# Optimization experiments

Measured on AMD Instinct MI355X. Metric: run time of the kernel, lower is better.

Reference implementation:

```python
import jax, jax.numpy as jnp
import numpy as np

B0, C0, H0, W0 = 2, 64, 48, 48
BR, DI, NS, RK, K = 128, 128, 16, 4, 4
EPS = 1e-5


def _bn_relu(x, g, b):
    # eval-mode BatchNorm2d (running mean 0, var 1) followed by ReLU; x is NCHW
    return jax.nn.relu(x * (g / jnp.sqrt(1.0 + EPS))[None, :, None, None] + b[None, :, None, None])


def _c1(x, w):
    # 1x1 conv, w: (O, C, 1, 1)
    return jnp.einsum('bchw,oc->bohw', x, w[:, :, 0, 0])


def _avgpool(x, k, s, p):
    # torch AvgPool2d with count_include_pad=True -> divide by k*k
    y = jax.lax.reduce_window(x, 0.0, jax.lax.add, (1, 1, k, k), (1, 1, s, s), ((0, 0), (0, 0), (p, p), (p, p)))
    return y / float(k * k)


def _resize(x, h, w):
    # bilinear, align_corners=False (half-pixel), NCHW
    return jax.image.resize(x, (x.shape[0], x.shape[1], h, w), 'bilinear')


def _pappm(x, s0_g, s0_b, s0_w, s1_g, s1_b, s1_w, s2_g, s2_b, s2_w, s3_g, s3_b, s3_w, s4_g, s4_b, s4_w, comp_g, comp_b, comp_w, sc_g, sc_b, sc_w):
    h, w = x.shape[2], x.shape[3]
    x0 = _c1(_bn_relu(x, s0_g, s0_b), s0_w)
    y1 = _c1(_bn_relu(_avgpool(x, 3, 1, 1), s1_g, s1_b), s1_w) + x0  # stride-1 pool keeps size
    y2 = _resize(_c1(_bn_relu(_avgpool(x, 5, 2, 2), s2_g, s2_b), s2_w), h, w) + x0
    y3 = _resize(_c1(_bn_relu(_avgpool(x, 9, 4, 4), s3_g, s3_b), s3_w), h, w) + x0
    y4 = _c1(_bn_relu(x.mean((2, 3), keepdims=True), s4_g, s4_b), s4_w) + x0  # 1x1 -> broadcast
    cat = jnp.concatenate([x0, y1, y2, y3, y4], axis=1)  # (B, 5*BR, H, W)
    comp = jax.lax.conv_general_dilated(_bn_relu(cat, comp_g, comp_b), comp_w, (1, 1), ((1, 1), (1, 1)), dimension_numbers=('NCHW', 'OIHW', 'NCHW'))
    return comp + _c1(_bn_relu(x, sc_g, sc_b), sc_w)


def _ss2d(xin, in_proj_w, dw_w, dw_b, x_proj_w, dt_w, dt_b, A_logs, Ds, ln_g, ln_b, out_proj_w):
    # xin: (B, H, W, d_model)
    Bb, Hh, Ww, _ = xin.shape
    xz = xin @ in_proj_w.T                      # (B,H,W,2*DI)
    xc, z = jnp.split(xz, 2, axis=-1)
    xc = jnp.transpose(xc, (0, 3, 1, 2))        # (B,DI,H,W)
    xc = jax.lax.conv_general_dilated(xc, dw_w, (1, 1), ((1, 1), (1, 1)), dimension_numbers=('NCHW', 'OIHW', 'NCHW'), feature_group_count=DI)
    xc = jax.nn.silu(xc + dw_b[None, :, None, None])
    L = Hh * Ww
    x_hw = xc.reshape(Bb, DI, L)
    x_wh = jnp.transpose(xc, (0, 1, 3, 2)).reshape(Bb, DI, L)
    xs = jnp.stack([x_hw, x_wh, x_hw[:, :, ::-1], x_wh[:, :, ::-1]], axis=1)  # (B,K,DI,L)
    x_dbl = jnp.einsum('bkdl,kcd->bkcl', xs, x_proj_w)
    dts, Bm, Cm = jnp.split(x_dbl, [RK, RK + NS], axis=2)  # (B,K,RK,L),(B,K,NS,L),(B,K,NS,L)
    delta = jax.nn.softplus(jnp.einsum('bkrl,kdr->bkdl', dts, dt_w) + dt_b[None, :, :, None])  # (B,K,DI,L)
    A = -jnp.exp(A_logs).reshape(K, DI, NS)
    a = jnp.exp(delta[..., None] * A[None, :, :, None, :])                    # (B,K,DI,L,NS)
    bu = (delta * xs)[..., None] * jnp.transpose(Bm, (0, 1, 3, 2))[:, :, None]  # (B,K,DI,L,NS)

    def comb(e1, e2):
        a1, b1 = e1
        a2, b2 = e2
        return a2 * a1, a2 * b1 + b2

    _, hst = jax.lax.associative_scan(comb, (a, bu), axis=3)  # h_t = a_t*h_{t-1} + b_t
    y = jnp.einsum('bkdln,bknl->bkdl', hst, Cm) + xs * Ds.reshape(K, DI)[None, :, :, None]
    inv = y[:, 2:4][:, :, :, ::-1]
    y3 = jnp.transpose(y[:, 1].reshape(Bb, DI, Ww, Hh), (0, 1, 3, 2)).reshape(Bb, DI, L)
    y4 = jnp.transpose(inv[:, 1].reshape(Bb, DI, Ww, Hh), (0, 1, 3, 2)).reshape(Bb, DI, L)
    ys = jnp.transpose(y[:, 0] + inv[:, 0] + y3 + y4, (0, 2, 1)).reshape(Bb, Hh, Ww, DI)
    mu = ys.mean(-1, keepdims=True)
    var = jnp.mean((ys - mu) ** 2, -1, keepdims=True)
    yn = (ys - mu) / jnp.sqrt(var + EPS) * ln_g + ln_b
    return (yn * jax.nn.silu(z)) @ out_proj_w.T  # (B,H,W,d_model)


def setup_inputs():
    key = jax.random.key(0)
    ks = iter(jax.random.split(key, 32))
    nrm = lambda shp, s: jax.random.normal(next(ks), shp, jnp.float32) * s
    d = {}
    d['x'] = nrm((B0, C0, H0, W0), 1.0)
    for nm in ['s0', 's1', 's2', 's3', 's4']:
        d[nm + '_g'] = jnp.ones((C0,), jnp.float32)
        d[nm + '_b'] = jnp.zeros((C0,), jnp.float32)
        d[nm + '_w'] = nrm((BR, C0, 1, 1), (2.0 / C0) ** 0.5)
    d['comp_g'] = jnp.ones((5 * BR,), jnp.float32)
    d['comp_b'] = jnp.zeros((5 * BR,), jnp.float32)
    d['comp_w'] = nrm((C0, 5 * BR, 3, 3), (2.0 / (5 * BR * 9)) ** 0.5)
    d['sc_g'] = jnp.ones((C0,), jnp.float32)
    d['sc_b'] = jnp.zeros((C0,), jnp.float32)
    d['sc_w'] = nrm((C0, C0, 1, 1), (2.0 / C0) ** 0.5)
    d['in_proj_w'] = nrm((2 * DI, C0), C0 ** -0.5)
    d['dw_w'] = nrm((DI, 1, 3, 3), 0.3)
    d['dw_b'] = jnp.zeros((DI,), jnp.float32)
    d['x_proj_w'] = nrm((K, RK + 2 * NS, DI), DI ** -0.5)
    d['dt_w'] = nrm((K, DI, RK), RK ** -0.5)
    d['dt_b'] = jnp.log(jnp.expm1(jnp.asarray(0.01, jnp.float32))) * jnp.ones((K, DI), jnp.float32)
    d['A_logs'] = jnp.tile(jnp.log(jnp.arange(1, NS + 1, dtype=jnp.float32))[None], (K * DI, 1))
    d['Ds'] = jnp.ones((K * DI,), jnp.float32)
    d['ln_g'] = jnp.ones((DI,), jnp.float32)
    d['ln_b'] = jnp.zeros((DI,), jnp.float32)
    d['out_proj_w'] = nrm((C0, DI), DI ** -0.5)
    d['fc1_w'] = nrm((BR, C0, 1, 1), C0 ** -0.5)
    d['fc1_b'] = jnp.zeros((BR,), jnp.float32)
    d['fc2_w'] = nrm((C0, BR, 1, 1), BR ** -0.5)
    d['fc2_b'] = jnp.zeros((C0,), jnp.float32)
    return d


def reference(x, s0_g, s0_b, s0_w, s1_g, s1_b, s1_w, s2_g, s2_b, s2_w, s3_g, s3_b, s3_w, s4_g, s4_b, s4_w, comp_g, comp_b, comp_w, sc_g, sc_b, sc_w, in_proj_w, dw_w, dw_b, x_proj_w, dt_w, dt_b, A_logs, Ds, ln_g, ln_b, out_proj_w, fc1_w, fc1_b, fc2_w, fc2_b):
    p = _pappm(x, s0_g, s0_b, s0_w, s1_g, s1_b, s1_w, s2_g, s2_b, s2_w, s3_g, s3_b, s3_w, s4_g, s4_b, s4_w, comp_g, comp_b, comp_w, sc_g, sc_b, sc_w)
    a = _ss2d(jnp.transpose(p, (0, 2, 3, 1)), in_proj_w, dw_w, dw_b, x_proj_w, dt_w, dt_b, A_logs, Ds, ln_g, ln_b, out_proj_w)
    x1 = jnp.transpose(a, (0, 3, 1, 2))  # (B,C0,H,W)
    h1 = jax.nn.silu(_c1(x1, fc1_w) + fc1_b[None, :, None, None])
    return _c1(h1, fc2_w) + fc2_b[None, :, None, None] + x1
```

## Files before the change

kernel.cpp:

```cpp
#include <hip/hip_runtime.h>
#include <math.h>

constexpr int cB = 2, cC = 64, cH = 48, cW = 48, cL = 48 * 48;
constexpr int cBR = 128, cDI = 128, cNS = 16, cRK = 4, cK = 4;
constexpr float cEPS = 1e-5f;
constexpr int NCH = 32;
constexpr int CHL = cL / NCH;
constexpr int KTOT = 5824;

typedef unsigned short u16;
typedef unsigned int u32;
typedef short s16x8 __attribute__((ext_vector_type(8)));
typedef float f32x4 __attribute__((ext_vector_type(4)));

__device__ __forceinline__ float bnrelu(float v, float g, float b) {
    float y = v * (g * rsqrtf(1.0f + cEPS)) + b;
    return y > 0.f ? y : 0.f;
}
__device__ __forceinline__ float silu(float v) {
    return v / (1.f + expf(-v));
}
__device__ __forceinline__ u16 f2bf(float f) {
    u32 u = __float_as_uint(f);
    u = (u + 0x7fffu + ((u >> 16) & 1u)) >> 16;
    return (u16)u;
}
__device__ __forceinline__ s16x8 cvt8(const float* p) {
    s16x8 r;
#pragma unroll
    for (int i = 0; i < 8; i++) r[i] = (short)f2bf(p[i]);
    return r;
}
__device__ __forceinline__ float row_sum16(float v) {
    v += __int_as_float(__builtin_amdgcn_update_dpp(0, __float_as_int(v), 0xB1, 0xF, 0xF, true));
    v += __int_as_float(__builtin_amdgcn_update_dpp(0, __float_as_int(v), 0x4E, 0xF, 0xF, true));
    v += __int_as_float(__builtin_amdgcn_update_dpp(0, __float_as_int(v), 0x124, 0xF, 0xF, true));
    v += __int_as_float(__builtin_amdgcn_update_dpp(0, __float_as_int(v), 0x128, 0xF, 0xF, true));
    return v;
}

__global__ void __launch_bounds__(256) k_pp(const float* __restrict__ x, float* __restrict__ pool3,
                                            float* __restrict__ pool5, float* __restrict__ pool9,
                                            float* __restrict__ gmean,
                                            const float* __restrict__ cw, const float* __restrict__ scw,
                                            const float* __restrict__ s0w, const float* __restrict__ s1w,
                                            const float* __restrict__ ipw, const float* __restrict__ xpw,
                                            const float* __restrict__ dww,
                                            u16* __restrict__ w8, u16* __restrict__ wcat,
                                            u16* __restrict__ ipk, u16* __restrict__ xpk,
                                            float* __restrict__ dwk) {
    __shared__ float sm[4];
    int blk = blockIdx.x;
    int t = threadIdx.x;
    if (blk < 1152) {
        int idx = blk * 256 + t;
        int w = idx % cW, h = (idx / cW) % cH, bc = idx / cL;
        const float* p = x + bc * cL;
        float s = 0.f;
        for (int dh = -1; dh <= 1; dh++) {
            int hh = h + dh; if (hh < 0 || hh >= cH) continue;
            for (int dw = -1; dw <= 1; dw++) {
                int ww = w + dw; if (ww < 0 || ww >= cW) continue;
                s += p[hh * cW + ww];
            }
        }
        pool3[idx] = s * (1.f / 9.f);
    } else if (blk < 1440) {
        int idx = (blk - 1152) * 256 + t;
        int w = idx % 24, h = (idx / 24) % 24, bc = idx / 576;
        const float* p = x + bc * cL;
        float s = 0.f;
        for (int kh = 0; kh < 5; kh++) {
            int hh = h * 2 - 2 + kh; if (hh < 0 || hh >= cH) continue;
            for (int kw = 0; kw < 5; kw++) {
                int ww = w * 2 - 2 + kw; if (ww < 0 || ww >= cW) continue;
                s += p[hh * cW + ww];
            }
        }
        pool5[idx] = s * (1.f / 25.f);
    } else if (blk < 1512) {
        int idx = (blk - 1440) * 256 + t;
        int w = idx % 12, h = (idx / 12) % 12, bc = idx / 144;
        const float* p = x + bc * cL;
        float s = 0.f;
        for (int kh = 0; kh < 9; kh++) {
            int hh = h * 4 - 4 + kh; if (hh < 0 || hh >= cH) continue;
            for (int kw = 0; kw < 9; kw++) {
                int ww = w * 4 - 4 + kw; if (ww < 0 || ww >= cW) continue;
                s += p[hh * cW + ww];
            }
        }
        pool9[idx] = s * (1.f / 81.f);
    } else if (blk < 1640) {
        int bc = blk - 1512;
        const float* p = x + bc * cL;
        float s = 0.f;
        for (int i = t; i < cL; i += 256) s += p[i];
        for (int m = 32; m > 0; m >>= 1) s += __shfl_down(s, m);
        if ((t & 63) == 0) sm[t >> 6] = s;
        __syncthreads();
        if (t == 0) gmean[bc] = (sm[0] + sm[1] + sm[2] + sm[3]) * (1.f / cL);
    } else if (blk < 3096) {
        int idx = (blk - 1640) * 256 + t;
        int o = idx / KTOT, kx = idx % KTOT;
        float v;
        if (kx < 5760) { int tap = kx / 640, ch = kx % 640; v = cw[(o * 640 + ch) * 9 + tap]; }
        else v = scw[o * 64 + (kx - 5760)];
        w8[(((size_t)(kx >> 3) * 64) + o) * 8 + (kx & 7)] = f2bf(v);
    } else if (blk < 3160) {
        int idx = (blk - 3096) * 256 + t;
        int g = idx >> 13, r = idx & 8191;
        int o = r >> 6, c = r & 63;
        float v = (g ? s1w : s0w)[r];
        int kt = c >> 5, q = (c >> 3) & 3, j = c & 7, nt = o >> 4, ln = o & 15;
        wcat[(size_t)((((g * 2 + kt) * 4 + q) * 8 + nt) * 16 + ln) * 8 + j] = f2bf(v);
    } else if (blk < 3224) {
        int idx = (blk - 3160) * 256 + t;
        int o = idx >> 6, c = idx & 63;
        int kt = c >> 5, q = (c >> 3) & 3, j = c & 7, nt = o >> 4, ln = o & 15;
        ipk[(size_t)(((kt * 4 + q) * 16 + nt) * 16 + ln) * 8 + j] = f2bf(ipw[idx]);
    } else if (blk < 3296) {
        int idx = (blk - 3224) * 256 + t;
        int o = idx >> 7, d = idx & 127;
        int kt = d >> 5, q = (d >> 3) & 3, j = d & 7, nt = o >> 4, ln = o & 15;
        xpk[(size_t)(((kt * 4 + q) * 9 + nt) * 16 + ln) * 8 + j] = f2bf(xpw[idx]);
    } else {
        int idx = (blk - 3296) * 256 + t;
        if (idx < 1152) {
            int tap = idx >> 7, ch = idx & 127;
            dwk[idx] = dww[ch * 9 + tap];
        }
    }
}

__global__ void __launch_bounds__(128) k_c1all(const float* __restrict__ pool5, const float* __restrict__ pool9,
                                               const float* __restrict__ gm,
                                               const float* __restrict__ s2g, const float* __restrict__ s2b,
                                               const float* __restrict__ s2w,
                                               const float* __restrict__ s3g, const float* __restrict__ s3b,
                                               const float* __restrict__ s3w,
                                               const float* __restrict__ s4g, const float* __restrict__ s4b,
                                               const float* __restrict__ s4w,
                                               float* __restrict__ c2cl, float* __restrict__ c3cl,
                                               float* __restrict__ c4) {
    int pos = blockIdx.x;
    const float *in, *g, *bb, *w;
    float* outp;
    int HW, b, pp;
    if (pos < cB * 576) { b = pos / 576; pp = pos % 576; in = pool5; g = s2g; bb = s2b; w = s2w; HW = 576; outp = c2cl + ((size_t)b * 576 + pp) * 128; }
    else if (pos < cB * 576 + cB * 144) { int r = pos - cB * 576; b = r / 144; pp = r % 144; in = pool9; g = s3g; bb = s3b; w = s3w; HW = 144; outp = c3cl + ((size_t)b * 144 + pp) * 128; }
    else { b = pos - cB * 576 - cB * 144; pp = 0; in = gm; g = s4g; bb = s4b; w = s4w; HW = 1; outp = c4 + (size_t)b * 128; }
    __shared__ float v[64];
    int t = threadIdx.x;
    if (t < 64) v[t] = bnrelu(in[(b * 64 + t) * HW + pp], g[t], bb[t]);
    __syncthreads();
    float acc = 0.f;
    const float* wr = w + t * 64;
#pragma unroll 16
    for (int c = 0; c < 64; c++) acc += v[c] * wr[c];
    outp[t] = acc;
}

__global__ void __launch_bounds__(512) k_cat2(
    const float* __restrict__ x, const float* __restrict__ pool3, const float* __restrict__ c4,
    const float* __restrict__ s0g, const float* __restrict__ s0b,
    const float* __restrict__ s1g, const float* __restrict__ s1b,
    const float* __restrict__ scg, const float* __restrict__ scb,
    const float* __restrict__ cg, const float* __restrict__ cbb,
    const u16* __restrict__ wcat, const float* __restrict__ c2cl, const float* __restrict__ c3cl,
    u16* __restrict__ catbf, u16* __restrict__ xbf) {
    int blk = blockIdx.x;
    int b = blk / 144;
    int l0 = (blk % 144) * 16;
    int t = threadIdx.x;
    __shared__ float axv[16][68];
    __shared__ float ap3[16][68];
    __shared__ u16 axc[16][66];
    int p = t & 15, c0 = t >> 4;
#pragma unroll
    for (int i = 0; i < 2; i++) {
        int c = i * 32 + c0;
        float xraw = x[(size_t)(b * 64 + c) * cL + l0 + p];
        float p3raw = pool3[(size_t)(b * 64 + c) * cL + l0 + p];
        axv[p][c] = bnrelu(xraw, s0g[c], s0b[c]);
        ap3[p][c] = bnrelu(p3raw, s1g[c], s1b[c]);
        axc[p][c] = f2bf(bnrelu(xraw, scg[c], scb[c]));
    }
    __syncthreads();
#pragma unroll
    for (int i = 0; i < 2; i++) {
        int idx = i * 512 + t;
        int pp = idx >> 6, cc = idx & 63;
        xbf[((size_t)b * cL + l0 + pp) * 64 + cc] = axc[pp][cc];
    }
    int wv = t >> 6, lane = t & 63, ln = lane & 15, q = lane >> 4;
    f32x4 ax = {};
    f32x4 ay = {};
#pragma unroll
    for (int kt = 0; kt < 2; kt++) {
        s16x8 a0 = cvt8(&axv[ln][kt * 32 + q * 8]);
        s16x8 a1 = cvt8(&ap3[ln][kt * 32 + q * 8]);
        s16x8 b0 = *(const s16x8*)(wcat + (size_t)((((0 * 2 + kt) * 4 + q) * 8 + wv) * 16 + ln) * 8);
        s16x8 b1 = *(const s16x8*)(wcat + (size_t)((((1 * 2 + kt) * 4 + q) * 8 + wv) * 16 + ln) * 8);
        ax = __builtin_amdgcn_mfma_f32_16x16x32_bf16(a0, b0, ax, 0, 0, 0);
        ay = __builtin_amdgcn_mfma_f32_16x16x32_bf16(a1, b1, ay, 0, 0, 0);
    }
    int hrow = l0 / cW, w0g = l0 % cW;
    float sy2 = hrow * 0.5f - 0.25f;
    float fy2 = floorf(sy2); int iy2 = (int)fy2; float ay2 = sy2 - fy2;
    int y20 = min(max(iy2, 0), 23), y21 = min(max(iy2 + 1, 0), 23);
    float sy3 = hrow * 0.25f - 0.375f;
    float fy3 = floorf(sy3); int iy3 = (int)fy3; float ay3 = sy3 - fy3;
    int y30 = min(max(iy3, 0), 11), y31 = min(max(iy3 + 1, 0), 11);
    const float* c2b = c2cl + (size_t)b * 576 * 128;
    const float* c3b = c3cl + (size_t)b * 144 * 128;
    int ch = wv * 16 + ln;
    float c4v = c4[b * 128 + ch];
#pragma unroll
    for (int r = 0; r < 4; r++) {
        int pp = q * 4 + r;
        int wq = w0g + pp;
        float sx2 = wq * 0.5f - 0.25f;
        float fx2 = floorf(sx2); int ix2 = (int)fx2; float ax2 = sx2 - fx2;
        int x20 = min(max(ix2, 0), 23), x21 = min(max(ix2 + 1, 0), 23);
        float sx3 = wq * 0.25f - 0.375f;
        float fx3 = floorf(sx3); int ix3 = (int)fx3; float ax3 = sx3 - fx3;
        int x30 = min(max(ix3, 0), 11), x31 = min(max(ix3 + 1, 0), 11);
        float v00 = c2b[(y20 * 24 + x20) * 128 + ch], v01 = c2b[(y20 * 24 + x21) * 128 + ch];
        float v10 = c2b[(y21 * 24 + x20) * 128 + ch], v11 = c2b[(y21 * 24 + x21) * 128 + ch];
        float t0 = v00 + (v01 - v00) * ax2, t1 = v10 + (v11 - v10) * ax2;
        float u2v = t0 + (t1 - t0) * ay2;
        float w00 = c3b[(y30 * 12 + x30) * 128 + ch], w01 = c3b[(y30 * 12 + x31) * 128 + ch];
        float w10 = c3b[(y31 * 12 + x30) * 128 + ch], w11 = c3b[(y31 * 12 + x31) * 128 + ch];
        float s0_ = w00 + (w01 - w00) * ax3, s1_ = w10 + (w11 - w10) * ax3;
        float u3v = s0_ + (s1_ - s0_) * ay3;
        float x0 = ax[r];
        float y1 = ay[r] + x0;
        float y2 = x0 + u2v;
        float y3 = x0 + u3v;
        float y4 = x0 + c4v;
        u16* base = catbf + ((size_t)b * cL + l0 + pp) * 640;
        base[ch]       = f2bf(bnrelu(x0, cg[ch],       cbb[ch]));
        base[128 + ch] = f2bf(bnrelu(y1, cg[128 + ch], cbb[128 + ch]));
        base[256 + ch] = f2bf(bnrelu(y2, cg[256 + ch], cbb[256 + ch]));
        base[384 + ch] = f2bf(bnrelu(y3, cg[384 + ch], cbb[384 + ch]));
        base[512 + ch] = f2bf(bnrelu(y4, cg[512 + ch], cbb[512 + ch]));
    }
}

__global__ void __launch_bounds__(512) k_compip(const u16* __restrict__ catbf,
                                                const u16* __restrict__ xbf,
                                                const u16* __restrict__ w8,
                                                const u16* __restrict__ ipk,
                                                float* __restrict__ xc, float* __restrict__ z) {
    int pix0 = blockIdx.x * 16;
    int b = pix0 / cL;
    int t = threadIdx.x;
    int wv = t >> 6, lane = t & 63, ln = lane & 15, q = lane >> 4;
    __shared__ float pl[8][16][68];
    __shared__ u16 pv16[16][72];
    int la = (pix0 + ln) - b * cL;
    int h = la / cW, w = la % cW;
    f32x4 acc[4] = {};
    int ks0 = wv * 23;
    int kcnt = (wv == 7) ? 21 : 23;
    for (int i = 0; i < kcnt; i++) {
        int ks = ks0 + i;
        s16x8 av;
        if (ks < 180) {
            int s = ks / 20;
            int cc = ks - s * 20;
            int s3 = s / 3;
            int kh = s3 - 1, kw = s - s3 * 3 - 1;
            int hh = h + kh, ww = w + kw;
            bool ok = (hh >= 0) && (hh < cH) && (ww >= 0) && (ww < cW);
            const u16* ap = catbf + (((size_t)b * cL + hh * cW + ww) * 640 + cc * 32 + q * 8);
            if (ok) av = *(const s16x8*)ap;
            else av = s16x8{0, 0, 0, 0, 0, 0, 0, 0};
        } else {
            int cc = ks - 180;
            av = *(const s16x8*)(xbf + (size_t)(pix0 + ln) * 64 + cc * 32 + q * 8);
        }
        const u16* wrow = w8 + ((size_t)ks * 4 + q) * 512;
#pragma unroll
        for (int j = 0; j < 4; j++) {
            s16x8 bv = *(const s16x8*)(wrow + (size_t)(j * 16 + ln) * 8);
            acc[j] = __builtin_amdgcn_mfma_f32_16x16x32_bf16(av, bv, acc[j], 0, 0, 0);
        }
    }
#pragma unroll
    for (int j = 0; j < 4; j++)
#pragma unroll
        for (int r = 0; r < 4; r++)
            pl[wv][q * 4 + r][j * 16 + ln] = acc[j][r];
    __syncthreads();
#pragma unroll
    for (int e = 0; e < 2; e++) {
        int id = e * 512 + t;
        int p = id >> 6, c = id & 63;
        float s = 0.f;
#pragma unroll
        for (int w2 = 0; w2 < 8; w2++) s += pl[w2][p][c];
        pv16[p][c] = f2bf(s);
    }
    __syncthreads();
    f32x4 a2[2] = {};
#pragma unroll
    for (int kt = 0; kt < 2; kt++) {
        s16x8 a = *(const s16x8*)(&pv16[ln][kt * 32 + q * 8]);
#pragma unroll
        for (int jn = 0; jn < 2; jn++) {
            int nt = wv * 2 + jn;
            s16x8 bfr = *(const s16x8*)(ipk + (size_t)(((kt * 4 + q) * 16 + nt) * 16 + ln) * 8);
            a2[jn] = __builtin_amdgcn_mfma_f32_16x16x32_bf16(a, bfr, a2[jn], 0, 0, 0);
        }
    }
#pragma unroll
    for (int jn = 0; jn < 2; jn++) {
        int o = (wv * 2 + jn) * 16 + ln;
#pragma unroll
        for (int r = 0; r < 4; r++) {
            int p = q * 4 + r;
            if (o < 128) xc[((size_t)pix0 + p) * 128 + o] = a2[jn][r];
            else         z[((size_t)pix0 + p) * 128 + (o - 128)] = a2[jn][r];
        }
    }
}

__global__ void __launch_bounds__(256) k_dw(const float* __restrict__ xc, const float* __restrict__ dwk,
                                            const float* __restrict__ dwb, float* __restrict__ xca) {
    int idx = blockIdx.x * 256 + threadIdx.x;
    int d4 = idx & 31;
    int rest = idx >> 5;
    int l = rest % cL, b = rest / cL;
    int h = l / cW, w = l % cW;
    const f32x4* xb = (const f32x4*)xc + (size_t)b * cL * 32;
    const f32x4* kb = (const f32x4*)dwk;
    f32x4 acc = ((const f32x4*)dwb)[d4];
#pragma unroll
    for (int i = 0; i < 3; i++) {
        int hh = h + i - 1; if (hh < 0 || hh >= cH) continue;
#pragma unroll
        for (int j = 0; j < 3; j++) {
            int ww = w + j - 1; if (ww < 0 || ww >= cW) continue;
            f32x4 v = xb[(size_t)(hh * cW + ww) * 32 + d4];
            f32x4 kv = kb[(i * 3 + j) * 32 + d4];
            acc += v * kv;
        }
    }
    f32x4 r;
#pragma unroll
    for (int c = 0; c < 4; c++) r[c] = silu(acc[c]);
    ((f32x4*)xca)[idx] = r;
}

__global__ void __launch_bounds__(1024) k_xdbl4(const float* __restrict__ xca, const u16* __restrict__ xpk,
                                                const float* __restrict__ dtw, const float* __restrict__ dtb,
                                                float* __restrict__ bc, float* __restrict__ delta) {
    int blk = blockIdx.x;
    int b = blk / 144;
    int l0 = (blk % 144) * 16;
    int t = threadIdx.x;
    __shared__ float av[16][132];
    __shared__ float Dt[16][148];
#pragma unroll
    for (int i = 0; i < 2; i++) {
        int id = i * 1024 + t;
        int d = id & 127, p = id >> 7;
        av[p][d] = xca[((size_t)b * cL + l0 + p) * 128 + d];
    }
    __syncthreads();
    int wv = t >> 6, lane = t & 63, ln = lane & 15, q = lane >> 4;
    if (wv < 9) {
        int nt = wv;
        f32x4 acc = {};
#pragma unroll
        for (int kt = 0; kt < 4; kt++) {
            s16x8 a = cvt8(&av[ln][kt * 32 + q * 8]);
            s16x8 bfr = *(const s16x8*)(xpk + (size_t)(((kt * 4 + q) * 9 + nt) * 16 + ln) * 8);
            acc = __builtin_amdgcn_mfma_f32_16x16x32_bf16(a, bfr, acc, 0, 0, 0);
        }
#pragma unroll
        for (int r = 0; r < 4; r++)
            Dt[q * 4 + r][nt * 16 + ln] = acc[r];
    }
    __syncthreads();
#pragma unroll
    for (int i = 0; i < 2; i++) {
        int id = i * 1024 + t;
        int cc = id & 31, kk = (id >> 5) & 3, p = id >> 7;
        bc[((size_t)(b * 4 + kk) * cL + l0 + p) * 32 + cc] = Dt[p][kk * 36 + 4 + cc];
    }
    {
        int d = t & 127;
        int kk = (t >> 7) & 3;
        int p0 = t >> 9;
        const float* wd = dtw + (size_t)(kk * 128 + d) * 4;
        float w0 = wd[0], w1 = wd[1], w2 = wd[2], w3 = wd[3];
        float bb = dtb[kk * 128 + d];
        float* dout = delta + ((size_t)(b * 4 + kk) * cL + l0) * 128 + d;
#pragma unroll
        for (int i = 0; i < 8; i++) {
            int p = p0 + i * 2;
            float pre = bb + w0 * Dt[p][kk * 36] + w1 * Dt[p][kk * 36 + 1]
                      + w2 * Dt[p][kk * 36 + 2] + w3 * Dt[p][kk * 36 + 3];
            float dl = pre > 20.f ? pre : log1pf(expf(pre));
            dout[(size_t)p * 128] = dl;
        }
    }
}

__device__ __forceinline__ int xs_index(int k, int l) {
    int lp = (k & 2) ? (cL - 1 - l) : l;
    if (k & 1) { int w = lp / cH, h = lp % cH; return h * cW + w; }
    return lp;
}

__global__ void __launch_bounds__(256) k_scan1(const float* __restrict__ delta, const float* __restrict__ xca,
                                               const float* __restrict__ bc, const float* __restrict__ Alogs,
                                               float* __restrict__ Pend, float* __restrict__ hend) {
    int blk = blockIdx.x;
    int c = blk & 31;
    if (c == NCH - 1) return;
    int g = blk >> 5;
    int dgq = g & 7, bk = g >> 3;
    int k = bk & 3, b = bk >> 2;
    int t = threadIdx.x;
    int n = t & 15;
    int d = dgq * 16 + (t >> 4);
    float A = -expf(Alogs[(k * 128 + d) * 16 + n]);
    const float* dp = delta + (size_t)bk * cL * 128 + d;
    const float* xp = xca + (size_t)b * cL * 128 + d;
    const float* bp = bc + (size_t)bk * cL * 32 + n;
    int off = xs_index(k, c * CHL);
    int step = (k == 0) ? 1 : (k == 1) ? cW : (k == 2) ? -1 : -cW;
    float P = 1.f, h = 0.f;
#pragma unroll 4
    for (int i = 0; i < CHL; i++) {
        float dl = dp[(size_t)off * 128];
        float a = expf(dl * A);
        h = a * h + dl * xp[(size_t)off * 128] * bp[(size_t)off * 32];
        P *= a;
        off += step;
        if (off >= cL) off -= (cL - 1);
        else if (off < 0) off += (cL - 1);
    }
    Pend[(size_t)blk * 256 + t] = P;
    hend[(size_t)blk * 256 + t] = h;
}

__global__ void __launch_bounds__(256) k_scan2(const float* __restrict__ Pend, float* __restrict__ hend) {
    int id = blockIdx.x * 256 + threadIdx.x;
    int t = id & 255;
    int g = id >> 8;
    float h = 0.f;
    for (int c = 0; c < NCH; c++) {
        size_t idx = ((size_t)g * NCH + c) * 256 + t;
        float tmp = hend[idx];
        float Pv = Pend[idx];
        hend[idx] = h;
        h = Pv * h + tmp;
    }
}

__global__ void __launch_bounds__(256) k_scan3(const float* __restrict__ delta, const float* __restrict__ xca,
                                               const float* __restrict__ bc, const float* __restrict__ Alogs,
                                               const float* __restrict__ Dsv, const float* __restrict__ hinb,
                                               float* __restrict__ y) {
    int blk = blockIdx.x;
    int c = blk & 31;
    int g = blk >> 5;
    int dgq = g & 7, bk = g >> 3;
    int k = bk & 3, b = bk >> 2;
    int t = threadIdx.x;
    int n = t & 15;
    int d = dgq * 16 + (t >> 4);
    float A = -expf(Alogs[(k * 128 + d) * 16 + n]);
    float Dsd = Dsv[k * 128 + d];
    const float* dp = delta + (size_t)bk * cL * 128 + d;
    const float* xp = xca + (size_t)b * cL * 128 + d;
    const float* bp = bc + (size_t)bk * cL * 32 + n;
    const float* cp = bc + (size_t)bk * cL * 32 + 16 + n;
    float* yb = y + (size_t)bk * cL * 128 + d;
    int off = xs_index(k, c * CHL);
    int step = (k == 0) ? 1 : (k == 1) ? cW : (k == 2) ? -1 : -cW;
    float h = hinb[(size_t)blk * 256 + t];
#pragma unroll 2
    for (int i = 0; i < CHL; i++) {
        float dl = dp[(size_t)off * 128];
        float xv = xp[(size_t)off * 128];
        float a = expf(dl * A);
        h = a * h + dl * xv * bp[(size_t)off * 32];
        float contrib = row_sum16(h * cp[(size_t)off * 32]);
        if (n == 0) yb[(size_t)off * 128] = contrib + xv * Dsd;
        off += step;
        if (off >= cL) off -= (cL - 1);
        else if (off < 0) off += (cL - 1);
    }
}

__global__ void __launch_bounds__(256) k_tail(const float* __restrict__ y, const float* __restrict__ z,
                                              const float* __restrict__ lng, const float* __restrict__ lnb,
                                              const float* __restrict__ opw,
                                              const float* __restrict__ f1w, const float* __restrict__ f1b,
                                              const float* __restrict__ f2w, const float* __restrict__ f2b,
                                              float* __restrict__ out) {
    int blk = blockIdx.x;
    int b = blk / 576;
    int l0 = (blk % 576) * 4;
    int t = threadIdx.x;
    __shared__ float v[4][132];
    __shared__ float x1s[4][68];
    __shared__ float h1s[4][132];
    __shared__ float mus[4], rss[4];
    const float* yb = y + (size_t)b * 4 * cL * 128;
#pragma unroll
    for (int i = 0; i < 2; i++) {
        int id = i * 256 + t;
        int d = id & 127, p = id >> 7;
        size_t base = (size_t)(l0 + p) * 128 + d;
        v[p][d] = yb[base] + yb[(size_t)cL * 128 + base] + yb[(size_t)2 * cL * 128 + base] + yb[(size_t)3 * cL * 128 + base];
    }
    __syncthreads();
    if (t < 64) {
        int p = t >> 4, c8 = (t & 15) * 8;
        float s = 0.f;
#pragma unroll
        for (int j = 0; j < 8; j++) s += v[p][c8 + j];
        s = row_sum16(s);
        float mu = s * (1.f / 128.f);
        float s2 = 0.f;
#pragma unroll
        for (int j = 0; j < 8; j++) { float dv = v[p][c8 + j] - mu; s2 += dv * dv; }
        s2 = row_sum16(s2);
        if ((t & 15) == 0) { mus[p] = mu; rss[p] = rsqrtf(s2 * (1.f / 128.f) + cEPS); }
    }
    __syncthreads();
#pragma unroll
    for (int i = 0; i < 2; i++) {
        int id = i * 256 + t;
        int d = id & 127, p = id >> 7;
        float zz = z[((size_t)b * cL + l0 + p) * 128 + d];
        v[p][d] = ((v[p][d] - mus[p]) * rss[p] * lng[d] + lnb[d]) * silu(zz);
    }
    __syncthreads();
    {
        int p = t & 3, o = t >> 2;
        const float* wr = opw + o * 128;
        float acc = 0.f;
#pragma unroll 16
        for (int d2 = 0; d2 < 128; d2++) acc += v[p][d2] * wr[d2];
        x1s[p][o] = acc;
    }
    __syncthreads();
#pragma unroll
    for (int i = 0; i < 2; i++) {
        int id = i * 256 + t;
        int p = id & 3, j = id >> 2;
        const float* wr = f1w + j * 64;
        float acc = f1b[j];
#pragma unroll 16
        for (int c = 0; c < 64; c++) acc += x1s[p][c] * wr[c];
        h1s[p][j] = silu(acc);
    }
    __syncthreads();
    {
        int p = t & 3, o = t >> 2;
        const float* wr = f2w + o * 128;
        float acc = f2b[o];
#pragma unroll 16
        for (int j = 0; j < 128; j++) acc += h1s[p][j] * wr[j];
        out[((size_t)b * 64 + o) * cL + l0 + p] = acc + x1s[p][o];
    }
}

extern "C" void kernel_launch(void* const* d_in, const int* in_sizes, int n_in,
                              void* d_out, int out_size, void* d_ws, size_t ws_size,
                              hipStream_t stream) {
    (void)in_sizes; (void)n_in; (void)out_size; (void)ws_size;
    const float* x    = (const float*)d_in[0];
    const float* s0g  = (const float*)d_in[1];
    const float* s0b  = (const float*)d_in[2];
    const float* s0w  = (const float*)d_in[3];
    const float* s1g  = (const float*)d_in[4];
    const float* s1b  = (const float*)d_in[5];
    const float* s1w  = (const float*)d_in[6];
    const float* s2g  = (const float*)d_in[7];
    const float* s2b  = (const float*)d_in[8];
    const float* s2w  = (const float*)d_in[9];
    const float* s3g  = (const float*)d_in[10];
    const float* s3b  = (const float*)d_in[11];
    const float* s3w  = (const float*)d_in[12];
    const float* s4g  = (const float*)d_in[13];
    const float* s4b  = (const float*)d_in[14];
    const float* s4w  = (const float*)d_in[15];
    const float* cg   = (const float*)d_in[16];
    const float* cbb  = (const float*)d_in[17];
    const float* cw   = (const float*)d_in[18];
    const float* scg  = (const float*)d_in[19];
    const float* scb  = (const float*)d_in[20];
    const float* scw  = (const float*)d_in[21];
    const float* ipw  = (const float*)d_in[22];
    const float* dww  = (const float*)d_in[23];
    const float* dwb  = (const float*)d_in[24];
    const float* xpw  = (const float*)d_in[25];
    const float* dtw  = (const float*)d_in[26];
    const float* dtb  = (const float*)d_in[27];
    const float* Alog = (const float*)d_in[28];
    const float* Dsv  = (const float*)d_in[29];
    const float* lng  = (const float*)d_in[30];
    const float* lnb  = (const float*)d_in[31];
    const float* opw  = (const float*)d_in[32];
    const float* f1w  = (const float*)d_in[33];
    const float* f1b  = (const float*)d_in[34];
    const float* f2w  = (const float*)d_in[35];
    const float* f2b  = (const float*)d_in[36];
    float* out = (float*)d_out;

    float* ws = (float*)d_ws;
    size_t off = 0;
    float* pool3  = ws + off; off += 294912;
    float* pool5  = ws + off; off += 73728;
    float* pool9  = ws + off; off += 18432;
    float* gmean  = ws + off; off += 128;
    float* c2cl   = ws + off; off += 147456;
    float* c3cl   = ws + off; off += 36864;
    float* c4     = ws + off; off += 256;
    u16*   catbf  = (u16*)(ws + off); off += 1474560;
    u16*   xbf    = (u16*)(ws + off); off += 147456;
    u16*   w8     = (u16*)(ws + off); off += 186368;
    u16*   wcat   = (u16*)(ws + off); off += 8192;
    u16*   ipk    = (u16*)(ws + off); off += 8192;
    float* xc     = ws + off; off += 589824;
    u16*   xpk    = (u16*)(ws + off); off += 9216;
    float* dwk    = ws + off; off += 1280;
    float* xca    = ws + off; off += 589824;
    float* zbuf   = ws + off; off += 589824;
    float* bcbuf  = ws + off; off += 589824;
    float* Pend   = ws + off; off += 524288;
    float* ybuf   = ws + off; off += 2359296;
    off += 294912;
    float* delta  = ws + 0;
    float* hend   = xc;

    k_pp<<<3301, 256, 0, stream>>>(x, pool3, pool5, pool9, gmean,
                                   cw, scw, s0w, s1w, ipw, xpw, dww,
                                   w8, wcat, ipk, xpk, dwk);
    k_c1all<<<cB * 576 + cB * 144 + cB, 128, 0, stream>>>(pool5, pool9, gmean, s2g, s2b, s2w,
                                                          s3g, s3b, s3w, s4g, s4b, s4w, c2cl, c3cl, c4);
    k_cat2<<<cB * 144, 512, 0, stream>>>(x, pool3, c4, s0g, s0b, s1g, s1b, scg, scb, cg, cbb,
                                         wcat, c2cl, c3cl, catbf, xbf);
    k_compip<<<cB * cL / 16, 512, 0, stream>>>(catbf, xbf, w8, ipk, xc, zbuf);
    k_dw<<<cB * cL * 128 / 4 / 256, 256, 0, stream>>>(xc, dwk, dwb, xca);
    k_xdbl4<<<cB * 144, 1024, 0, stream>>>(xca, xpk, dtw, dtb, bcbuf, delta);
    k_scan1<<<64 * NCH, 256, 0, stream>>>(delta, xca, bcbuf, Alog, Pend, hend);
    k_scan2<<<64, 256, 0, stream>>>(Pend, hend);
    k_scan3<<<64 * NCH, 256, 0, stream>>>(delta, xca, bcbuf, Alog, Dsv, hend, ybuf);
    k_tail<<<cB * 576, 256, 0, stream>>>(ybuf, zbuf, lng, lnb, opw, f1w, f1b, f2w, f2b, out);
}
```

Before: 288.1 us.

## Fuse 3x3 avgpool into cat kernel and use MFMA for pooled 1x1 convs

```diff
diff --git a/kernel.cpp b/kernel.cpp
--- a/kernel.cpp
+++ b/kernel.cpp
@@ -39,34 +39,22 @@
     return v;
 }
 
-__global__ void __launch_bounds__(256) k_pp(const float* __restrict__ x, float* __restrict__ pool3,
+__global__ void __launch_bounds__(256) k_pp(const float* __restrict__ x,
                                             float* __restrict__ pool5, float* __restrict__ pool9,
                                             float* __restrict__ gmean,
                                             const float* __restrict__ cw, const float* __restrict__ scw,
                                             const float* __restrict__ s0w, const float* __restrict__ s1w,
                                             const float* __restrict__ ipw, const float* __restrict__ xpw,
                                             const float* __restrict__ dww,
+                                            const float* __restrict__ s2w, const float* __restrict__ s3w,
                                             u16* __restrict__ w8, u16* __restrict__ wcat,
                                             u16* __restrict__ ipk, u16* __restrict__ xpk,
-                                            float* __restrict__ dwk) {
+                                            float* __restrict__ dwk, u16* __restrict__ c1k) {
     __shared__ float sm[4];
     int blk = blockIdx.x;
     int t = threadIdx.x;
-    if (blk < 1152) {
+    if (blk < 288) {
         int idx = blk * 256 + t;
-        int w = idx % cW, h = (idx / cW) % cH, bc = idx / cL;
-        const float* p = x + bc * cL;
-        float s = 0.f;
-        for (int dh = -1; dh <= 1; dh++) {
-            int hh = h + dh; if (hh < 0 || hh >= cH) continue;
-            for (int dw = -1; dw <= 1; dw++) {
-                int ww = w + dw; if (ww < 0 || ww >= cW) continue;
-                s += p[hh * cW + ww];
-            }
-        }
-        pool3[idx] = s * (1.f / 9.f);
-    } else if (blk < 1440) {
-        int idx = (blk - 1152) * 256 + t;
         int w = idx % 24, h = (idx / 24) % 24, bc = idx / 576;
         const float* p = x + bc * cL;
         float s = 0.f;
@@ -78,8 +66,8 @@
             }
         }
         pool5[idx] = s * (1.f / 25.f);
-    } else if (blk < 1512) {
-        int idx = (blk - 1440) * 256 + t;
+    } else if (blk < 360) {
+        int idx = (blk - 288) * 256 + t;
         int w = idx % 12, h = (idx / 12) % 12, bc = idx / 144;
         const float* p = x + bc * cL;
         float s = 0.f;
@@ -91,8 +79,8 @@
             }
         }
         pool9[idx] = s * (1.f / 81.f);
-    } else if (blk < 1640) {
-        int bc = blk - 1512;
+    } else if (blk < 488) {
+        int bc = blk - 360;
         const float* p = x + bc * cL;
         float s = 0.f;
         for (int i = t; i < cL; i += 256) s += p[i];
@@ -100,69 +88,105 @@
         if ((t & 63) == 0) sm[t >> 6] = s;
         __syncthreads();
         if (t == 0) gmean[bc] = (sm[0] + sm[1] + sm[2] + sm[3]) * (1.f / cL);
-    } else if (blk < 3096) {
-        int idx = (blk - 1640) * 256 + t;
+    } else if (blk < 1944) {
+        int idx = (blk - 488) * 256 + t;
         int o = idx / KTOT, kx = idx % KTOT;
         float v;
         if (kx < 5760) { int tap = kx / 640, ch = kx % 640; v = cw[(o * 640 + ch) * 9 + tap]; }
         else v = scw[o * 64 + (kx - 5760)];
         w8[(((size_t)(kx >> 3) * 64) + o) * 8 + (kx & 7)] = f2bf(v);
-    } else if (blk < 3160) {
-        int idx = (blk - 3096) * 256 + t;
+    } else if (blk < 2008) {
+        int idx = (blk - 1944) * 256 + t;
         int g = idx >> 13, r = idx & 8191;
         int o = r >> 6, c = r & 63;
         float v = (g ? s1w : s0w)[r];
         int kt = c >> 5, q = (c >> 3) & 3, j = c & 7, nt = o >> 4, ln = o & 15;
         wcat[(size_t)((((g * 2 + kt) * 4 + q) * 8 + nt) * 16 + ln) * 8 + j] = f2bf(v);
-    } else if (blk < 3224) {
-        int idx = (blk - 3160) * 256 + t;
+    } else if (blk < 2072) {
+        int idx = (blk - 2008) * 256 + t;
         int o = idx >> 6, c = idx & 63;
         int kt = c >> 5, q = (c >> 3) & 3, j = c & 7, nt = o >> 4, ln = o & 15;
         ipk[(size_t)(((kt * 4 + q) * 16 + nt) * 16 + ln) * 8 + j] = f2bf(ipw[idx]);
-    } else if (blk < 3296) {
-        int idx = (blk - 3224) * 256 + t;
+    } else if (blk < 2144) {
+        int idx = (blk - 2072) * 256 + t;
         int o = idx >> 7, d = idx & 127;
         int kt = d >> 5, q = (d >> 3) & 3, j = d & 7, nt = o >> 4, ln = o & 15;
         xpk[(size_t)(((kt * 4 + q) * 9 + nt) * 16 + ln) * 8 + j] = f2bf(xpw[idx]);
-    } else {
-        int idx = (blk - 3296) * 256 + t;
+    } else if (blk < 2149) {
+        int idx = (blk - 2144) * 256 + t;
         if (idx < 1152) {
             int tap = idx >> 7, ch = idx & 127;
             dwk[idx] = dww[ch * 9 + tap];
         }
-    }
-}
-
-__global__ void __launch_bounds__(128) k_c1all(const float* __restrict__ pool5, const float* __restrict__ pool9,
-                                               const float* __restrict__ gm,
-                                               const float* __restrict__ s2g, const float* __restrict__ s2b,
-                                               const float* __restrict__ s2w,
-                                               const float* __restrict__ s3g, const float* __restrict__ s3b,
-                                               const float* __restrict__ s3w,
-                                               const float* __restrict__ s4g, const float* __restrict__ s4b,
-                                               const float* __restrict__ s4w,
-                                               float* __restrict__ c2cl, float* __restrict__ c3cl,
-                                               float* __restrict__ c4) {
-    int pos = blockIdx.x;
-    const float *in, *g, *bb, *w;
+    } else {
+        int idx = (blk - 2149) * 256 + t;
+        int g = idx >> 13, r = idx & 8191;
+        int o = r >> 6, c = r & 63;
+        float v = (g ? s3w : s2w)[r];
+        int kt = c >> 5, q = (c >> 3) & 3, j = c & 7, nt = o >> 4, ln = o & 15;
+        c1k[(size_t)((((g * 2 + kt) * 4 + q) * 8 + nt) * 16 + ln) * 8 + j] = f2bf(v);
+    }
+}
+
+__global__ void __launch_bounds__(256) k_c1m(const float* __restrict__ pool5, const float* __restrict__ pool9,
+                                             const float* __restrict__ gm,
+                                             const float* __restrict__ s2g, const float* __restrict__ s2b,
+                                             const float* __restrict__ s3g, const float* __restrict__ s3b,
+                                             const float* __restrict__ s4g, const float* __restrict__ s4b,
+                                             const float* __restrict__ s4w, const u16* __restrict__ c1k,
+                                             float* __restrict__ c2cl, float* __restrict__ c3cl,
+                                             float* __restrict__ c4) {
+    int blk = blockIdx.x, t = threadIdx.x;
+    if (blk >= 90) {
+        int b = blk - 90;
+        __shared__ float v[64];
+        if (t < 64) v[t] = bnrelu(gm[b * 64 + t], s4g[t], s4b[t]);
+        __syncthreads();
+        if (t < 128) {
+            const float* wr = s4w + t * 64;
+            float acc = 0.f;
+#pragma unroll 16
+            for (int c = 0; c < 64; c++) acc += v[c] * wr[c];
+            c4[b * 128 + t] = acc;
+        }
+        return;
+    }
+    int set, b, pp0, HW;
+    const float *in, *g, *bb;
     float* outp;
-    int HW, b, pp;
-    if (pos < cB * 576) { b = pos / 576; pp = pos % 576; in = pool5; g = s2g; bb = s2b; w = s2w; HW = 576; outp = c2cl + ((size_t)b * 576 + pp) * 128; }
-    else if (pos < cB * 576 + cB * 144) { int r = pos - cB * 576; b = r / 144; pp = r % 144; in = pool9; g = s3g; bb = s3b; w = s3w; HW = 144; outp = c3cl + ((size_t)b * 144 + pp) * 128; }
-    else { b = pos - cB * 576 - cB * 144; pp = 0; in = gm; g = s4g; bb = s4b; w = s4w; HW = 1; outp = c4 + (size_t)b * 128; }
-    __shared__ float v[64];
-    int t = threadIdx.x;
-    if (t < 64) v[t] = bnrelu(in[(b * 64 + t) * HW + pp], g[t], bb[t]);
-    __syncthreads();
-    float acc = 0.f;
-    const float* wr = w + t * 64;
-#pragma unroll 16
-    for (int c = 0; c < 64; c++) acc += v[c] * wr[c];
-    outp[t] = acc;
+    if (blk < 72) { set = 0; b = blk / 36; pp0 = (blk % 36) * 16; HW = 576; in = pool5; g = s2g; bb = s2b; outp = c2cl + (size_t)b * 576 * 128; }
+    else { int r = blk - 72; set = 1; b = r / 9; pp0 = (r % 9) * 16; HW = 144; in = pool9; g = s3g; bb = s3b; outp = c3cl + (size_t)b * 144 * 128; }
+    __shared__ u16 av16[16][72];
+#pragma unroll
+    for (int i = 0; i < 4; i++) {
+        int id = i * 256 + t;
+        int c = id >> 4, p = id & 15;
+        av16[p][c] = f2bf(bnrelu(in[(size_t)(b * 64 + c) * HW + pp0 + p], g[c], bb[c]));
+    }
+    __syncthreads();
+    int wv = t >> 6, lane = t & 63, ln = lane & 15, q = lane >> 4;
+    f32x4 acc[2] = {};
+#pragma unroll
+    for (int kt = 0; kt < 2; kt++) {
+        s16x8 a = *(const s16x8*)(&av16[ln][kt * 32 + q * 8]);
+#pragma unroll
+        for (int jn = 0; jn < 2; jn++) {
+            int nt = wv * 2 + jn;
+            s16x8 bfr = *(const s16x8*)(c1k + (size_t)((((set * 2 + kt) * 4 + q) * 8 + nt) * 16 + ln) * 8);
+            acc[jn] = __builtin_amdgcn_mfma_f32_16x16x32_bf16(a, bfr, acc[jn], 0, 0, 0);
+        }
+    }
+#pragma unroll
+    for (int jn = 0; jn < 2; jn++) {
+        int o = (wv * 2 + jn) * 16 + ln;
+#pragma unroll
+        for (int r = 0; r < 4; r++)
+            outp[(size_t)(pp0 + q * 4 + r) * 128 + o] = acc[jn][r];
+    }
 }
 
 __global__ void __launch_bounds__(512) k_cat2(
-    const float* __restrict__ x, const float* __restrict__ pool3, const float* __restrict__ c4,
+    const float* __restrict__ x, const float* __restrict__ c4,
     const float* __restrict__ s0g, const float* __restrict__ s0b,
     const float* __restrict__ s1g, const float* __restrict__ s1b,
     const float* __restrict__ scg, const float* __restrict__ scb,
@@ -172,19 +196,39 @@
     int blk = blockIdx.x;
     int b = blk / 144;
     int l0 = (blk % 144) * 16;
+    int hrow = l0 / cW, w0g = l0 % cW;
     int t = threadIdx.x;
+    __shared__ float xst[64][3][19];
     __shared__ float axv[16][68];
     __shared__ float ap3[16][68];
     __shared__ u16 axc[16][66];
-    int p = t & 15, c0 = t >> 4;
+#pragma unroll
+    for (int i = 0; i < 7; i++) {
+        int id = i * 512 + t;
+        if (id < 3456) {
+            int c = id / 54, rem = id % 54, rw = rem / 18, wi = rem % 18;
+            int hh = hrow + rw - 1, ww = w0g + wi - 1;
+            float v = 0.f;
+            if (hh >= 0 && hh < cH && ww >= 0 && ww < cW)
+                v = x[(size_t)(b * 64 + c) * cL + hh * cW + ww];
+            xst[c][rw][wi] = v;
+        }
+    }
+    __syncthreads();
 #pragma unroll
     for (int i = 0; i < 2; i++) {
-        int c = i * 32 + c0;
-        float xraw = x[(size_t)(b * 64 + c) * cL + l0 + p];
-        float p3raw = pool3[(size_t)(b * 64 + c) * cL + l0 + p];
-        axv[p][c] = bnrelu(xraw, s0g[c], s0b[c]);
-        ap3[p][c] = bnrelu(p3raw, s1g[c], s1b[c]);
-        axc[p][c] = f2bf(bnrelu(xraw, scg[c], scb[c]));
+        int id = i * 512 + t;
+        int c = id >> 4, p = id & 15;
+        float xv = xst[c][1][p + 1];
+        float s9 = 0.f;
+#pragma unroll
+        for (int rw = 0; rw < 3; rw++)
+#pragma unroll
+            for (int wi = 0; wi < 3; wi++)
+                s9 += xst[c][rw][p + wi];
+        axv[p][c] = bnrelu(xv, s0g[c], s0b[c]);
+        ap3[p][c] = bnrelu(s9 * (1.f / 9.f), s1g[c], s1b[c]);
+        axc[p][c] = f2bf(bnrelu(xv, scg[c], scb[c]));
     }
     __syncthreads();
 #pragma unroll
@@ -205,7 +249,6 @@
         ax = __builtin_amdgcn_mfma_f32_16x16x32_bf16(a0, b0, ax, 0, 0, 0);
         ay = __builtin_amdgcn_mfma_f32_16x16x32_bf16(a1, b1, ay, 0, 0, 0);
     }
-    int hrow = l0 / cW, w0g = l0 % cW;
     float sy2 = hrow * 0.5f - 0.25f;
     float fy2 = floorf(sy2); int iy2 = (int)fy2; float ay2 = sy2 - fy2;
     int y20 = min(max(iy2, 0), 23), y21 = min(max(iy2 + 1, 0), 23);
@@ -619,7 +662,6 @@
 
     float* ws = (float*)d_ws;
     size_t off = 0;
-    float* pool3  = ws + off; off += 294912;
     float* pool5  = ws + off; off += 73728;
     float* pool9  = ws + off; off += 18432;
     float* gmean  = ws + off; off += 128;
@@ -631,6 +673,8 @@
     u16*   w8     = (u16*)(ws + off); off += 186368;
     u16*   wcat   = (u16*)(ws + off); off += 8192;
     u16*   ipk    = (u16*)(ws + off); off += 8192;
+    u16*   c1k    = (u16*)(ws + off); off += 8192;
+    if (off < 2359296) off = 2359296;
     float* xc     = ws + off; off += 589824;
     u16*   xpk    = (u16*)(ws + off); off += 9216;
     float* dwk    = ws + off; off += 1280;
@@ -643,12 +687,12 @@
     float* delta  = ws + 0;
     float* hend   = xc;
 
-    k_pp<<<3301, 256, 0, stream>>>(x, pool3, pool5, pool9, gmean,
-                                   cw, scw, s0w, s1w, ipw, xpw, dww,
-                                   w8, wcat, ipk, xpk, dwk);
-    k_c1all<<<cB * 576 + cB * 144 + cB, 128, 0, stream>>>(pool5, pool9, gmean, s2g, s2b, s2w,
-                                                          s3g, s3b, s3w, s4g, s4b, s4w, c2cl, c3cl, c4);
-    k_cat2<<<cB * 144, 512, 0, stream>>>(x, pool3, c4, s0g, s0b, s1g, s1b, scg, scb, cg, cbb,
+    k_pp<<<2213, 256, 0, stream>>>(x, pool5, pool9, gmean,
+                                   cw, scw, s0w, s1w, ipw, xpw, dww, s2w, s3w,
+                                   w8, wcat, ipk, xpk, dwk, c1k);
+    k_c1m<<<92, 256, 0, stream>>>(pool5, pool9, gmean, s2g, s2b, s3g, s3b, s4g, s4b, s4w,
+                                  c1k, c2cl, c3cl, c4);
+    k_cat2<<<cB * 144, 512, 0, stream>>>(x, c4, s0g, s0b, s1g, s1b, scg, scb, cg, cbb,
                                          wcat, c2cl, c3cl, catbf, xbf);
     k_compip<<<cB * cL / 16, 512, 0, stream>>>(catbf, xbf, w8, ipk, xc, zbuf);
     k_dw<<<cB * cL * 128 / 4 / 256, 256, 0, stream>>>(xc, dwk, dwb, xca);
```

Result: no change. 290.6 us (+0.9%).
